# Kernel tuning notes

Hardware: AMD Instinct MI355X
Metric: run time of the kernel (lower is better)

The kernel has to match this reference:

```python
import jax, jax.numpy as jnp
import numpy as np

P1 = np.array([[1000.0, 0.0, 128.0, 64000.0],
               [0.0, 1000.0, 128.0, 64000.0],
               [0.0, 0.0, 1.0, 500.0]])
P2 = np.array([[-128.0, 0.0, 1000.0, 64000.0],
               [-128.0, 1000.0, 0.0, 64000.0],
               [-1.0, 0.0, 0.0, 500.0]])


def calculate_fundamental_matrix(P_src, P_dst):
    # l2 = F21 @ x1 : maps a point in P_src onto a line in P_dst
    C1 = -np.linalg.inv(P_src[:3, :3]) @ P_src[:3, 3]
    e = P_dst @ np.append(C1, 1.0)          # epipole of src camera center in dst view
    return np.cross(e, np.eye(3) * -1) @ P_dst @ np.linalg.pinv(P_src)


def setup_inputs() -> dict:
    key = jax.random.key(0)
    view1 = jax.random.normal(key, (8, 4, 256, 256), dtype=jnp.float32)
    F21 = calculate_fundamental_matrix(P1, P2).astype(np.float32)
    return {"view1": view1, "F": jnp.asarray(F21)}


def reference(view1, F):
    """Epipolar image translation: out(x2) = line integral of view1 along the
    epipolar line l1 = F^T @ x2 (bilinear sampling in v, unit steps in u,
    zero outside the image). Matches fume_torch_lib.translate semantics."""
    B, C, H, W = view1.shape
    dt = view1.dtype
    F = F.astype(dt)
    ys = jnp.arange(H, dtype=dt)[:, None]   # (H,1)
    xs = jnp.arange(W, dtype=dt)[None, :]   # (1,W)
    # line coefficients l = F^T @ [x, y, 1], per output pixel -> (H,W)
    a = F[0, 0] * xs + F[1, 0] * ys + F[2, 0]
    b = F[0, 1] * xs + F[1, 1] * ys + F[2, 1]
    c = F[0, 2] * xs + F[1, 2] * ys + F[2, 2]
    n = jnp.sqrt(a * a + b * b) + jnp.asarray(1e-12, dt)
    a, b, c = a / n, b / n, c / n
    ok = (jnp.abs(b) > 1e-6).astype(dt)                 # drop near-vertical lines
    b_safe = jnp.where(jnp.abs(b) > 1e-6, b, jnp.asarray(1.0, dt))

    def step(acc, u):
        uf = u.astype(dt)
        v = -(a * uf + c) / b_safe                      # (H,W) source row per out pixel
        v0 = jnp.floor(v)
        f = v - v0
        i0 = v0.astype(jnp.int32)
        i1 = i0 + 1
        m0 = ((i0 >= 0) & (i0 < H)).astype(dt)
        m1 = ((i1 >= 0) & (i1 < H)).astype(dt)
        col = jax.lax.dynamic_index_in_dim(view1, u, axis=3, keepdims=False)  # (B,C,H)
        s0 = col[:, :, jnp.clip(i0, 0, H - 1)]          # (B,C,H,W)
        s1 = col[:, :, jnp.clip(i1, 0, H - 1)]
        val = (s0 * (1.0 - f) * m0 + s1 * f * m1) * ok
        return acc + val, None

    out, _ = jax.lax.scan(step, jnp.zeros_like(view1), jnp.arange(W))
    return out
```

## Files before the change

### kernel.cpp

```cpp
#include <hip/hip_runtime.h>
#include <cstdint>

constexpr int Hh = 256, Ww = 256, BCc = 32;
constexpr int RBLK = 35;
constexpr int USTRIDE = RBLK * BCc * 8 * 2;
constexpr int UPLANES = 264;

typedef _Float16 half2v  __attribute__((ext_vector_type(2)));
typedef _Float16 half8v  __attribute__((ext_vector_type(8)));
typedef __fp16   fp16x2  __attribute__((ext_vector_type(2)));
typedef float    float4v __attribute__((ext_vector_type(4)));
typedef uint32_t uint4v  __attribute__((ext_vector_type(4)));

static __device__ inline half2v pack2(float a, float b) {
    fp16x2 r = __builtin_amdgcn_cvt_pkrtz(a, b);
    return __builtin_bit_cast(half2v, r);
}

__global__ __launch_bounds__(256) void fume_pack(const float* __restrict__ in,
                                                 char* __restrict__ T4) {
    const int t   = threadIdx.x;
    const int bid = blockIdx.x;
    if (bid >= 128) {
        constexpr int NA = UPLANES * 3 * 32;
        constexpr int NB = 8 * 32 * 32;
        for (int id = (bid - 128) * 256 + t; id < NA + NB; id += 8 * 256) {
            int u, blk, ch;
            if (id < NA) {
                u = id / 96;
                int rem = id - u * 96;
                int bsel = rem >> 5;
                blk = (bsel == 0) ? 0 : (bsel == 1 ? 33 : 34);
                ch = rem & 31;
            } else {
                int id2 = id - NA;
                u = 256 + (id2 >> 10);
                int rem = id2 & 1023;
                blk = 1 + (rem >> 5);
                ch = rem & 31;
            }
            uint4v z = {0, 0, 0, 0};
            *(uint4v*)(T4 + (size_t)u * USTRIDE + blk * 512 + ch * 16) = z;
        }
        return;
    }
    __shared__ float tile[32][65];
    const int chg = bid >> 5;
    const int r0  = ((bid >> 2) & 7) * 32;
    const int u0  = (bid & 3) * 64;

    for (int ci = 0; ci < 8; ++ci) {
        int ch = chg * 8 + ci;
#pragma unroll
        for (int it = 0; it < 8; ++it) {
            int idx = it * 256 + t;
            tile[idx >> 6][idx & 63] =
                in[ch * (Hh * Ww) + (r0 + (idx >> 6)) * Ww + u0 + (idx & 63)];
        }
        __syncthreads();
        int u_l = t >> 2, rs = (t & 3) * 8;
        uint32_t w[4];
#pragma unroll
        for (int j = 0; j < 4; ++j) {
            half2v p = pack2(tile[rs + 2 * j][u_l], tile[rs + 2 * j + 1][u_l]);
            __builtin_memcpy(&w[j], &p, 4);
        }
        int blk = ((r0 + rs) >> 3) + 1;
        uint4v val = {w[0], w[1], w[2], w[3]};
        *(uint4v*)(T4 + (size_t)(u0 + u_l) * USTRIDE + blk * 512 + ch * 16) = val;
        __syncthreads();
    }
}

__global__ __launch_bounds__(256, 8) void fume_mfma(const char* __restrict__ T4,
                                                    const float* __restrict__ Fm,
                                                    float* __restrict__ out) {
    __shared__ float red1[2][16][32];
    __shared__ float red2[2][16][32];
    const int t    = threadIdx.x;
    const int lane = t & 63;
    const int wv   = t >> 6;
    const int uh   = wv & 1;
    const int ly   = wv >> 1;
    const int px   = lane & 15;
    const int quad = lane >> 4;
    const int x0   = ((int)blockIdx.x & 15) * 16;
    const int y    = ((int)blockIdx.x >> 4) * 2 + ly;
    const int x    = x0 + px;

    float xf = (float)x, yf = (float)y;
    float a = Fm[0] * xf + Fm[3] * yf + Fm[6];
    float b = Fm[1] * xf + Fm[4] * yf + Fm[7];
    float c = Fm[2] * xf + Fm[5] * yf + Fm[8];
    float n = sqrtf(a * a + b * b) + 1e-12f;
    a /= n; b /= n; c /= n;

    float alpha, beta_i;
    int u_lo, u_hi;
    if (fabsf(b) > 1e-6f) {
        alpha  = -a / b;
        beta_i = -c / b + 8.f;
        u_lo = 0; u_hi = Ww - 1;
        if (fabsf(alpha) > 1e-12f) {
            float inv = 1.f / alpha;
            float t0 = (7.f - beta_i) * inv;
            float t1 = (264.f - beta_i) * inv;
            int lo = (int)floorf(fminf(t0, t1));
            int hi = (int)ceilf (fmaxf(t0, t1));
            u_lo = lo > 0 ? lo : 0;
            u_hi = hi < (Ww - 1) ? hi : (Ww - 1);
        } else if (beta_i <= 7.f || beta_i >= 264.f) {
            u_lo = 1 << 20; u_hi = -(1 << 20);
        }
    } else {
        alpha = 0.f; beta_i = 3.0e4f;
        u_lo = 1 << 20; u_hi = -(1 << 20);
    }

    float xA = (float)x0, xB = (float)(x0 + 15);
    float aA = Fm[0] * xA + Fm[3] * yf + Fm[6];
    float bA = Fm[1] * xA + Fm[4] * yf + Fm[7];
    float cA = Fm[2] * xA + Fm[5] * yf + Fm[8];
    float aB = Fm[0] * xB + Fm[3] * yf + Fm[6];
    float bB = Fm[1] * xB + Fm[4] * yf + Fm[7];
    float cB = Fm[2] * xB + Fm[5] * yf + Fm[8];
    float alA = -aA / bA, beA = -cA / bA + 8.f;
    float alB = -aB / bB, beB = -cB / bB + 8.f;

    int lo = u_lo, hi = u_hi;
#pragma unroll
    for (int off = 1; off < 64; off <<= 1) {
        int l2 = __shfl_xor(lo, off, 64);
        int h2 = __shfl_xor(hi, off, 64);
        lo = lo < l2 ? lo : l2;
        hi = hi > h2 ? hi : h2;
    }
    lo = __builtin_amdgcn_readfirstlane(lo);
    hi = __builtin_amdgcn_readfirstlane(hi);

    float4v acc0 = {0.f, 0.f, 0.f, 0.f};
    float4v acc1 = {0.f, 0.f, 0.f, 0.f};

    if (lo <= hi) {
        int len = hi - lo + 1;
        int h0  = (((len + 1) >> 1) + 7) & ~7;
        int us, ngroups;
        if (uh == 0) { us = lo; ngroups = h0 >> 3; }
        else {
            int rem = len - h0;
            us = lo + h0;
            ngroups = rem > 0 ? ((((rem + 1) >> 1) + 3) >> 2) : 0;
        }

        float v   = fmaf(alpha, (float)(us + (quad >> 1)), beta_i);
        float a2  = 2.f * alpha, a8 = 8.f * alpha;
        float vA0 = fmaf(alA, (float)us, beA);
        float vB0 = fmaf(alB, (float)us, beB);
        float aA8 = 8.f * alA, aB8 = 8.f * alB;
        float mnA = fminf(7.f * alA, 0.f);
        float mnB = fminf(7.f * alB, 0.f);
        float lane8 = (float)((quad & 1) * 8);
        const int lane_fix = (quad >> 1) * USTRIDE + (quad & 1) * 512 + px * 16;
        const char* pb = T4 + (size_t)us * USTRIDE + lane_fix;

        const half2v one2  = {(_Float16)1.f, (_Float16)1.f};
        const half2v zero2 = {(_Float16)0.f, (_Float16)0.f};

        for (int g = 0; g < ngroups; ++g) {
            float mn = fminf(vA0 + mnA, vB0 + mnB);
            float Mf = floorf(fmaf(mn, 0.125f, -0.125f));
            Mf = fmaxf(0.f, fminf(Mf, 33.f));
            const char* pg = pb + ((int)Mf << 9);
            float w0 = fmaf(Mf, -8.f, v) - lane8;

#pragma unroll
            for (int i = 0; i < 4; ++i) {
                float wi = fmaf((float)i, a2, w0);
                uint4v b0 = *(const uint4v*)(pg);
                uint4v b1 = *(const uint4v*)(pg + 256);
                half2v vb2 = pack2(wi, wi);
                uint32_t aw[4];
#pragma unroll
                for (int j = 0; j < 4; ++j) {
                    half2v cj = {(_Float16)(float)(2 * j),
                                 (_Float16)(float)(2 * j + 1)};
                    half2v d  = vb2 - cj;
                    half2v ad = __builtin_elementwise_abs(d);
                    half2v tj = __builtin_elementwise_max(one2 - ad, zero2);
                    __builtin_memcpy(&aw[j], &tj, 4);
                }
                half8v A;
                __builtin_memcpy(&A, aw, 16);
                half8v B0 = __builtin_bit_cast(half8v, b0);
                half8v B1 = __builtin_bit_cast(half8v, b1);
                acc0 = __builtin_amdgcn_mfma_f32_16x16x32_f16(A, B0, acc0, 0, 0, 0);
                acc1 = __builtin_amdgcn_mfma_f32_16x16x32_f16(A, B1, acc1, 0, 0, 0);
                pg += 2 * USTRIDE;
            }
            v += a8; vA0 += aA8; vB0 += aB8; pb += 8 * USTRIDE;
        }
    }

    if (uh == 1) {
#pragma unroll
        for (int r = 0; r < 4; ++r) {
            int pm = quad * 4 + r;
            red1[ly][pm][(px + pm) & 31]      = acc0[r];
            red1[ly][pm][(px + 16 + pm) & 31] = acc1[r];
        }
    }
    __syncthreads();
    if (uh == 0) {
#pragma unroll
        for (int r = 0; r < 4; ++r) {
            int pm = quad * 4 + r;
            red2[ly][pm][(px + pm) & 31] =
                acc0[r] + red1[ly][pm][(px + pm) & 31];
            red2[ly][pm][(px + 16 + pm) & 31] =
                acc1[r] + red1[ly][pm][(px + 16 + pm) & 31];
        }
    }
    __syncthreads();
    {
        int ly2 = t >> 7, s = t & 127, pxs = s & 15, cg = s >> 4;
        int yy = ((int)blockIdx.x >> 4) * 2 + ly2;
#pragma unroll
        for (int j = 0; j < 4; ++j) {
            int ch = cg * 4 + j;
            float val = red2[ly2][pxs][(ch + pxs) & 31];
            out[(size_t)ch * (Hh * Ww) + yy * Ww + x0 + pxs] = val;
        }
    }
}

__global__ __launch_bounds__(256) void fume_fallback(const float* __restrict__ src,
                                                     const float* __restrict__ Fm,
                                                     float* __restrict__ out) {
    int g = blockIdx.x * 256 + threadIdx.x;
    int part = g & 3;
    int pix  = g >> 2;
    int x = pix & (Ww - 1);
    int y = pix >> 8;
    int ch0 = part * 8;
    float xf = (float)x, yf = (float)y;
    float a = Fm[0] * xf + Fm[3] * yf + Fm[6];
    float b = Fm[1] * xf + Fm[4] * yf + Fm[7];
    float c = Fm[2] * xf + Fm[5] * yf + Fm[8];
    float n = sqrtf(a * a + b * b) + 1e-12f;
    a /= n; b /= n; c /= n;
    float acc[8];
#pragma unroll
    for (int k = 0; k < 8; ++k) acc[k] = 0.f;
    if (fabsf(b) > 1e-6f) {
        float alpha = -a / b, beta = -c / b;
        for (int u = 0; u < Ww; ++u) {
            float v  = fmaf(alpha, (float)u, beta);
            float rf = floorf(v);
            float f  = v - rf;
            int   ri = (int)rf;
            float w0 = ((unsigned)ri       < (unsigned)Hh) ? (1.f - f) : 0.f;
            float w1 = ((unsigned)(ri + 1) < (unsigned)Hh) ? f         : 0.f;
            int r0 = ri < 0 ? 0 : (ri > Hh - 1 ? Hh - 1 : ri);
            int r1 = ri + 1 < 0 ? 0 : (ri + 1 > Hh - 1 ? Hh - 1 : ri + 1);
#pragma unroll
            for (int k = 0; k < 8; ++k) {
                float s0 = src[(size_t)(ch0 + k) * (Hh * Ww) + r0 * Ww + u];
                float s1 = src[(size_t)(ch0 + k) * (Hh * Ww) + r1 * Ww + u];
                acc[k] = fmaf(w0, s0, fmaf(w1, s1, acc[k]));
            }
        }
    }
#pragma unroll
    for (int k = 0; k < 8; ++k)
        out[(size_t)(ch0 + k) * (Hh * Ww) + pix] = acc[k];
}

extern "C" void kernel_launch(void* const* d_in, const int* in_sizes, int n_in,
                              void* d_out, int out_size, void* d_ws, size_t ws_size,
                              hipStream_t stream) {
    const float* view1 = (const float*)d_in[0];
    const float* Fm    = (const float*)d_in[1];
    float* out = (float*)d_out;

    constexpr size_t t4_bytes = (size_t)UPLANES * USTRIDE;
    if (ws_size >= t4_bytes) {
        char* T4 = (char*)d_ws;
        fume_pack<<<136, 256, 0, stream>>>(view1, T4);
        fume_mfma<<<2048, 256, 0, stream>>>(T4, Fm, out);
    } else {
        fume_fallback<<<(Hh * Ww * 4) / 256, 256, 0, stream>>>(view1, Fm, out);
    }
}
```

Baseline: 104.5 us.

## Switch to 32x32x16 MFMA with four-wave u-split and re-tiled pack kernel

The main kernel now gives each block one output row of 32 pixels and uses the 32x32x16 f16 MFMA instead of pairs of 16x16x32 MFMAs. The u range is split across four waves, which are summed through LDS at the end. The row-block offset is recomputed per u step with a wave-uniform readfirstlane instead of once per group of eight. The pack kernel is re-tiled into 512 blocks that each load 8 channels by 8 rows by 64 columns with one sync, and launch bounds for the main kernel drop from 8 to 4 blocks per CU. The intent is fewer MFMA instructions, a narrower B-operand footprint and more pack parallelism, at the cost of more per-step scalar work and lower occupancy.

Result: faster. 99.30 us (-5.0%).

```diff
diff --git a/kernel.cpp b/kernel.cpp
--- a/kernel.cpp
+++ b/kernel.cpp
@@ -6,11 +6,11 @@
 constexpr int USTRIDE = RBLK * BCc * 8 * 2;
 constexpr int UPLANES = 264;
 
-typedef _Float16 half2v  __attribute__((ext_vector_type(2)));
-typedef _Float16 half8v  __attribute__((ext_vector_type(8)));
-typedef __fp16   fp16x2  __attribute__((ext_vector_type(2)));
-typedef float    float4v __attribute__((ext_vector_type(4)));
-typedef uint32_t uint4v  __attribute__((ext_vector_type(4)));
+typedef _Float16 half2v   __attribute__((ext_vector_type(2)));
+typedef _Float16 half8v   __attribute__((ext_vector_type(8)));
+typedef __fp16   fp16x2   __attribute__((ext_vector_type(2)));
+typedef float    float16v __attribute__((ext_vector_type(16)));
+typedef uint32_t uint4v   __attribute__((ext_vector_type(4)));
 
 static __device__ inline half2v pack2(float a, float b) {
     fp16x2 r = __builtin_amdgcn_cvt_pkrtz(a, b);
@@ -21,10 +21,10 @@
                                                  char* __restrict__ T4) {
     const int t   = threadIdx.x;
     const int bid = blockIdx.x;
-    if (bid >= 128) {
+    if (bid >= 512) {
         constexpr int NA = UPLANES * 3 * 32;
         constexpr int NB = 8 * 32 * 32;
-        for (int id = (bid - 128) * 256 + t; id < NA + NB; id += 8 * 256) {
+        for (int id = (bid - 512) * 256 + t; id < NA + NB; id += 8 * 256) {
             int u, blk, ch;
             if (id < NA) {
                 u = id / 96;
@@ -44,48 +44,47 @@
         }
         return;
     }
-    __shared__ float tile[32][65];
-    const int chg = bid >> 5;
-    const int r0  = ((bid >> 2) & 7) * 32;
-    const int u0  = (bid & 3) * 64;
-
-    for (int ci = 0; ci < 8; ++ci) {
-        int ch = chg * 8 + ci;
-#pragma unroll
-        for (int it = 0; it < 8; ++it) {
-            int idx = it * 256 + t;
-            tile[idx >> 6][idx & 63] =
-                in[ch * (Hh * Ww) + (r0 + (idx >> 6)) * Ww + u0 + (idx & 63)];
-        }
-        __syncthreads();
-        int u_l = t >> 2, rs = (t & 3) * 8;
+    __shared__ float lds[8][8][65];
+    const int chg = bid & 3;
+    const int r0  = ((bid >> 2) & 31) * 8;
+    const int u0  = (bid >> 7) * 64;
+    const int blk = (r0 >> 3) + 1;
+
+#pragma unroll
+    for (int it = 0; it < 16; ++it) {
+        int idx = it * 256 + t;
+        int ch = idx >> 9, rr = (idx >> 6) & 7, uu = idx & 63;
+        lds[ch][rr][uu] =
+            in[(chg * 8 + ch) * (Hh * Ww) + (r0 + rr) * Ww + u0 + uu];
+    }
+    __syncthreads();
+    const int chl = t & 7;
+#pragma unroll
+    for (int p = 0; p < 2; ++p) {
+        int u_l = (t >> 3) + p * 32;
         uint32_t w[4];
 #pragma unroll
         for (int j = 0; j < 4; ++j) {
-            half2v p = pack2(tile[rs + 2 * j][u_l], tile[rs + 2 * j + 1][u_l]);
-            __builtin_memcpy(&w[j], &p, 4);
-        }
-        int blk = ((r0 + rs) >> 3) + 1;
+            half2v pr = pack2(lds[chl][2 * j][u_l], lds[chl][2 * j + 1][u_l]);
+            __builtin_memcpy(&w[j], &pr, 4);
+        }
         uint4v val = {w[0], w[1], w[2], w[3]};
-        *(uint4v*)(T4 + (size_t)(u0 + u_l) * USTRIDE + blk * 512 + ch * 16) = val;
-        __syncthreads();
-    }
-}
-
-__global__ __launch_bounds__(256, 8) void fume_mfma(const char* __restrict__ T4,
+        *(uint4v*)(T4 + (size_t)(u0 + u_l) * USTRIDE + blk * 512
+                   + (chg * 8 + chl) * 16) = val;
+    }
+}
+
+__global__ __launch_bounds__(256, 4) void fume_mfma(const char* __restrict__ T4,
                                                     const float* __restrict__ Fm,
                                                     float* __restrict__ out) {
-    __shared__ float red1[2][16][32];
-    __shared__ float red2[2][16][32];
+    __shared__ float red[4][32][33];
     const int t    = threadIdx.x;
     const int lane = t & 63;
-    const int wv   = t >> 6;
-    const int uh   = wv & 1;
-    const int ly   = wv >> 1;
-    const int px   = lane & 15;
-    const int quad = lane >> 4;
-    const int x0   = ((int)blockIdx.x & 15) * 16;
-    const int y    = ((int)blockIdx.x >> 4) * 2 + ly;
+    const int wq   = t >> 6;
+    const int px   = lane & 31;
+    const int h    = lane >> 5;
+    const int x0   = ((int)blockIdx.x & 7) * 32;
+    const int y    = (int)blockIdx.x >> 3;
     const int x    = x0 + px;
 
     float xf = (float)x, yf = (float)y;
@@ -117,7 +116,7 @@
         u_lo = 1 << 20; u_hi = -(1 << 20);
     }
 
-    float xA = (float)x0, xB = (float)(x0 + 15);
+    float xA = (float)x0, xB = (float)(x0 + 31);
     float aA = Fm[0] * xA + Fm[3] * yf + Fm[6];
     float bA = Fm[1] * xA + Fm[4] * yf + Fm[7];
     float cA = Fm[2] * xA + Fm[5] * yf + Fm[8];
@@ -138,47 +137,38 @@
     lo = __builtin_amdgcn_readfirstlane(lo);
     hi = __builtin_amdgcn_readfirstlane(hi);
 
-    float4v acc0 = {0.f, 0.f, 0.f, 0.f};
-    float4v acc1 = {0.f, 0.f, 0.f, 0.f};
+    float16v acc = {0.f, 0.f, 0.f, 0.f, 0.f, 0.f, 0.f, 0.f,
+                    0.f, 0.f, 0.f, 0.f, 0.f, 0.f, 0.f, 0.f};
 
     if (lo <= hi) {
         int len = hi - lo + 1;
-        int h0  = (((len + 1) >> 1) + 7) & ~7;
-        int us, ngroups;
-        if (uh == 0) { us = lo; ngroups = h0 >> 3; }
-        else {
-            int rem = len - h0;
-            us = lo + h0;
-            ngroups = rem > 0 ? ((((rem + 1) >> 1) + 3) >> 2) : 0;
-        }
-
-        float v   = fmaf(alpha, (float)(us + (quad >> 1)), beta_i);
-        float a2  = 2.f * alpha, a8 = 8.f * alpha;
-        float vA0 = fmaf(alA, (float)us, beA);
-        float vB0 = fmaf(alB, (float)us, beB);
-        float aA8 = 8.f * alA, aB8 = 8.f * alB;
-        float mnA = fminf(7.f * alA, 0.f);
-        float mnB = fminf(7.f * alB, 0.f);
-        float lane8 = (float)((quad & 1) * 8);
-        const int lane_fix = (quad >> 1) * USTRIDE + (quad & 1) * 512 + px * 16;
-        const char* pb = T4 + (size_t)us * USTRIDE + lane_fix;
+        int C   = (len + 3) >> 2;
+        int cq  = (C + 3) >> 2;
+        int nit = C - wq * cq;
+        nit = nit < 0 ? 0 : (nit > cq ? cq : nit);
+        int us  = lo + wq * cq * 4;
+
+        float v  = fmaf(alpha, (float)us, beta_i);
+        float vA = fmaf(alA, (float)us, beA);
+        float vB = fmaf(alB, (float)us, beB);
+        float l8h = (float)(8 * h);
+        const char* pu = T4 + (size_t)us * USTRIDE + (h << 9) + (px << 4);
 
         const half2v one2  = {(_Float16)1.f, (_Float16)1.f};
         const half2v zero2 = {(_Float16)0.f, (_Float16)0.f};
 
-        for (int g = 0; g < ngroups; ++g) {
-            float mn = fminf(vA0 + mnA, vB0 + mnB);
-            float Mf = floorf(fmaf(mn, 0.125f, -0.125f));
-            Mf = fmaxf(0.f, fminf(Mf, 33.f));
-            const char* pg = pb + ((int)Mf << 9);
-            float w0 = fmaf(Mf, -8.f, v) - lane8;
-
+        for (int it = 0; it < nit; ++it) {
 #pragma unroll
             for (int i = 0; i < 4; ++i) {
-                float wi = fmaf((float)i, a2, w0);
-                uint4v b0 = *(const uint4v*)(pg);
-                uint4v b1 = *(const uint4v*)(pg + 256);
-                half2v vb2 = pack2(wi, wi);
+                float mnu = fminf(vA, vB);
+                float Mf  = floorf(fmaf(mnu, 0.125f, -0.125f));
+                Mf = fmaxf(0.f, fminf(Mf, 33.f));
+                int Mo = (int)Mf << 9;
+                Mo = __builtin_amdgcn_readfirstlane(Mo);
+                uint4v bw = *(const uint4v*)(pu + Mo);
+
+                float vbl = fmaf(Mf, -8.f, v) - l8h;
+                half2v vb2 = pack2(vbl, vbl);
                 uint32_t aw[4];
 #pragma unroll
                 for (int j = 0; j < 4; ++j) {
@@ -191,44 +181,28 @@
                 }
                 half8v A;
                 __builtin_memcpy(&A, aw, 16);
-                half8v B0 = __builtin_bit_cast(half8v, b0);
-                half8v B1 = __builtin_bit_cast(half8v, b1);
-                acc0 = __builtin_amdgcn_mfma_f32_16x16x32_f16(A, B0, acc0, 0, 0, 0);
-                acc1 = __builtin_amdgcn_mfma_f32_16x16x32_f16(A, B1, acc1, 0, 0, 0);
-                pg += 2 * USTRIDE;
+                half8v B = __builtin_bit_cast(half8v, bw);
+                acc = __builtin_amdgcn_mfma_f32_32x32x16_f16(A, B, acc, 0, 0, 0);
+
+                v += alpha; vA += alA; vB += alB; pu += USTRIDE;
             }
-            v += a8; vA0 += aA8; vB0 += aB8; pb += 8 * USTRIDE;
-        }
-    }
-
-    if (uh == 1) {
-#pragma unroll
-        for (int r = 0; r < 4; ++r) {
-            int pm = quad * 4 + r;
-            red1[ly][pm][(px + pm) & 31]      = acc0[r];
-            red1[ly][pm][(px + 16 + pm) & 31] = acc1[r];
-        }
-    }
-    __syncthreads();
-    if (uh == 0) {
-#pragma unroll
-        for (int r = 0; r < 4; ++r) {
-            int pm = quad * 4 + r;
-            red2[ly][pm][(px + pm) & 31] =
-                acc0[r] + red1[ly][pm][(px + pm) & 31];
-            red2[ly][pm][(px + 16 + pm) & 31] =
-                acc1[r] + red1[ly][pm][(px + 16 + pm) & 31];
-        }
+        }
+    }
+
+#pragma unroll
+    for (int r = 0; r < 16; ++r) {
+        int m = (r & 3) + 8 * (r >> 2) + 4 * h;
+        red[wq][m][px] = acc[r];
     }
     __syncthreads();
     {
-        int ly2 = t >> 7, s = t & 127, pxs = s & 15, cg = s >> 4;
-        int yy = ((int)blockIdx.x >> 4) * 2 + ly2;
-#pragma unroll
-        for (int j = 0; j < 4; ++j) {
-            int ch = cg * 4 + j;
-            float val = red2[ly2][pxs][(ch + pxs) & 31];
-            out[(size_t)ch * (Hh * Ww) + yy * Ww + x0 + pxs] = val;
+        int pxs = t & 31, cg = t >> 5;
+#pragma unroll
+        for (int jj = 0; jj < 4; ++jj) {
+            int ch = cg + 8 * jj;
+            float val = red[0][pxs][ch] + red[1][pxs][ch]
+                      + red[2][pxs][ch] + red[3][pxs][ch];
+            out[(size_t)ch * (Hh * Ww) + y * Ww + x0 + pxs] = val;
         }
     }
 }
@@ -285,7 +259,7 @@
     constexpr size_t t4_bytes = (size_t)UPLANES * USTRIDE;
     if (ws_size >= t4_bytes) {
         char* T4 = (char*)d_ws;
-        fume_pack<<<136, 256, 0, stream>>>(view1, T4);
+        fume_pack<<<520, 256, 0, stream>>>(view1, T4);
         fume_mfma<<<2048, 256, 0, stream>>>(T4, Fm, out);
     } else {
         fume_fallback<<<(Hh * Ww * 4) / 256, 256, 0, stream>>>(view1, Fm, out);
```
